# Kernel tuning notes

Hardware: AMD Instinct MI355X
Metric: run time of the kernel (lower is better)

## Reference

```python
import jax, jax.numpy as jnp
import numpy as np

T = 64      # sequence_length / rolling_size
B = 256     # batch
XD = 128    # x_dim
HD = 1024   # h_dim
SKIP = 5    # frozen skip_size (torch code draws random.randint(1,10) at init)


def _make_masks(rs, n):
    # Mirrors: W1=randint(0,1); W2=1 if W1==0 else randint(0,1)
    masks = []
    for _ in range(n):
        w1 = int(rs.randint(0, 2))
        w2 = 1 if w1 == 0 else int(rs.randint(0, 2))
        masks.append((float(w1), float(w2)))
    return masks

_RS = np.random.RandomState(0)
ENC_MASKS = _make_masks(_RS, T)  # encoder constructed first in RAE.__init__
DEC_MASKS = _make_masks(_RS, T)


def _gru_cell(x, h, W_ih, W_hh, b_ih, b_hh):
    # torch.nn.GRUCell semantics
    gi = x @ W_ih.T + b_ih            # [B, 3H]
    gh = h @ W_hh.T + b_hh            # [B, 3H]
    i_r, i_z, i_n = jnp.split(gi, 3, axis=1)
    h_r, h_z, h_n = jnp.split(gh, 3, axis=1)
    r = jax.nn.sigmoid(i_r + h_r)
    z = jax.nn.sigmoid(i_z + h_z)
    n = jnp.tanh(i_n + r * h_n)
    return (1.0 - z) * n + z * h


def setup_inputs() -> dict:
    key = jax.random.key(0)
    ks = jax.random.split(key, 12)
    s = 0.05
    return {
        "input": jax.random.normal(ks[0], (B, T, XD), jnp.float32),
        "enc_W_ih": jax.random.normal(ks[1], (3 * HD, XD), jnp.float32) * s,
        "enc_W_hh": jax.random.normal(ks[2], (3 * HD, HD), jnp.float32) * s,
        "enc_b_ih": jax.random.normal(ks[3], (3 * HD,), jnp.float32) * s,
        "enc_b_hh": jax.random.normal(ks[4], (3 * HD,), jnp.float32) * s,
        "dec_W_ih": jax.random.normal(ks[5], (3 * HD, XD), jnp.float32) * s,
        "dec_W_hh": jax.random.normal(ks[6], (3 * HD, HD), jnp.float32) * s,
        "dec_b_ih": jax.random.normal(ks[7], (3 * HD,), jnp.float32) * s,
        "dec_b_hh": jax.random.normal(ks[8], (3 * HD,), jnp.float32) * s,
        "lin_W": jax.random.normal(ks[9], (XD, HD), jnp.float32) * s,
        "lin_b": jax.random.normal(ks[10], (XD,), jnp.float32) * s,
    }


def reference(input, enc_W_ih, enc_W_hh, enc_b_ih, enc_b_hh,
              dec_W_ih, dec_W_hh, dec_b_ih, dec_b_hh, lin_W, lin_b):
    Bn = input.shape[0]
    zeros_h = jnp.zeros((Bn, HD), input.dtype)

    # ---- Encoder: masked-skip GRU recurrence (list semantics match torch) ----
    h_origs = [zeros_h]
    h_skips = [zeros_h] * SKIP
    for i in range(T):
        h_prev = h_origs[i] * ENC_MASKS[i][0] + h_skips[i - SKIP] * ENC_MASKS[i][1]
        h_new = _gru_cell(input[:, i], h_prev, enc_W_ih, enc_W_hh, enc_b_ih, enc_b_hh)
        h_origs.append(h_new)
        h_skips.append(h_new)  # chunk(repeat(1,2)) gives two identical copies
    h_enc = h_origs[-1] + h_skips[-1]

    # ---- Decoder: feeds back its own projected output ----
    GO = jnp.zeros((Bn, XD), input.dtype)
    h_origs = [h_enc]
    h_skips = [zeros_h] * SKIP
    outputs = []
    for i in range(T):
        x_in = GO if i == 0 else outputs[i - 1]
        h_prev = h_origs[i] * DEC_MASKS[i][0] + h_skips[i - SKIP] * DEC_MASKS[i][1]
        h_new = _gru_cell(x_in, h_prev, dec_W_ih, dec_W_hh, dec_b_ih, dec_b_hh)
        h_origs.append(h_new)
        h_skips.append(h_new)
        # torch projects AFTER the appends, using h_origs[i] (pre-update state)
        proj = (h_origs[i] + h_skips[i - SKIP]) @ lin_W.T + lin_b
        outputs.append(proj)

    return jnp.stack(outputs, axis=1)  # [B, T, XD], matches permute(1,0,2)
```

## Files before the change

### kernel.cpp

```cpp
#include <hip/hip_runtime.h>
#include <cstdint>
#include <cstddef>

#define XDIM 128
#define HDIM 1024
#define ORS 8192

typedef __attribute__((ext_vector_type(8))) short short8;
typedef __attribute__((ext_vector_type(4))) float f32x4;

static const size_t GSTRIDE = (size_t)36 * 64 * 64 * 8;
static const size_t EPACK   = 4 * GSTRIDE;

__device__ __forceinline__ unsigned short f2bf(float f) {
  union { float f; unsigned u; } c; c.f = f;
  unsigned u = c.u + (0x7fffu + ((c.u >> 16) & 1u));
  return (unsigned short)(u >> 16);
}
__device__ __forceinline__ float sigm_(float x) { return 1.f / (1.f + __expf(-x)); }
__device__ __forceinline__ float tanh_(float x) { return 2.f / (1.f + __expf(-2.f * x)) - 1.f; }

__device__ __forceinline__ short8 cvt8(float4 a, float4 b) {
  short8 o;
  o[0] = (short)f2bf(a.x); o[1] = (short)f2bf(a.y); o[2] = (short)f2bf(a.z); o[3] = (short)f2bf(a.w);
  o[4] = (short)f2bf(b.x); o[5] = (short)f2bf(b.y); o[6] = (short)f2bf(b.z); o[7] = (short)f2bf(b.w);
  return o;
}

__global__ __launch_bounds__(256) void pack_gates(
    const float* __restrict__ eWih, const float* __restrict__ eWhh,
    const float* __restrict__ dWih, const float* __restrict__ dWhh,
    short* __restrict__ Bg)
{
  unsigned t = blockIdx.x * 256u + threadIdx.x;
  unsigned l  = t & 63u; t >>= 6;
  unsigned nf = t & 63u; t >>= 6;
  unsigned ks = t % 36u; t /= 36u;
  unsigned g  = t & 3u;  t >>= 2;
  if (t >= 2u) return;
  if ((g == 2u && ks >= 4u) || (g == 3u && ks < 4u)) return;
  const float* Wih = t ? dWih : eWih;
  const float* Whh = t ? dWhh : eWhh;
  int k = (int)(ks * 32u + (l >> 4) * 8u);
  int n = (int)(nf * 16u + (l & 15u));
  const float* src;
  if (g == 3u)      src = Whh + (size_t)(2048 + n) * HDIM + (k - XDIM);
  else if (g == 2u) src = Wih + (size_t)(2048 + n) * XDIM + k;
  else if (ks < 4u) src = Wih + (size_t)(g * HDIM + n) * XDIM + k;
  else              src = Whh + (size_t)(g * HDIM + n) * HDIM + (k - XDIM);
  float4 a = *(const float4*)src;
  float4 b = *(const float4*)(src + 4);
  size_t off = ((((size_t)t * 4u + g) * 36u + ks) * 64u + nf) * 64u + l;
  *(short8*)(Bg + off * 8u) = cvt8(a, b);
}

__global__ __launch_bounds__(256) void pack_lin(const float* __restrict__ linW,
                                                short* __restrict__ Bl)
{
  unsigned t = blockIdx.x * 256u + threadIdx.x;
  unsigned l  = t & 63u; t >>= 6;
  unsigned nf = t & 7u;  t >>= 3;
  unsigned ks = t;
  if (ks >= 32u) return;
  int k = (int)(ks * 32u + (l >> 4) * 8u);
  int n = (int)(nf * 16u + (l & 15u));
  const float* src = linW + (size_t)n * HDIM + k;
  float4 a = *(const float4*)src;
  float4 b = *(const float4*)(src + 4);
  *(short8*)(Bl + (((size_t)ks * 8u + nf) * 64u + l) * 8u) = cvt8(a, b);
}

__global__ __launch_bounds__(256) void pack_bias(
    const float* __restrict__ eIh, const float* __restrict__ eHh,
    const float* __restrict__ dIh, const float* __restrict__ dHh,
    float* __restrict__ bias)
{
  unsigned t = blockIdx.x * 256u + threadIdx.x;
  if (t >= 8192u) return;
  unsigned n = t & 1023u, g = (t >> 10) & 3u, e = t >> 12;
  const float* bih = e ? dIh : eIh;
  const float* bhh = e ? dHh : eHh;
  float v;
  if (g == 0u)      v = bih[n] + bhh[n];
  else if (g == 1u) v = bih[HDIM + n] + bhh[HDIM + n];
  else if (g == 2u) v = bih[2 * HDIM + n];
  else              v = bhh[2 * HDIM + n];
  bias[t] = v;
}

__global__ __launch_bounds__(256) void pack_x(const float* __restrict__ in,
                                              unsigned short* __restrict__ Xe)
{
  unsigned t = blockIdx.x * 256u + threadIdx.x;
  unsigned row = t & 255u; t >>= 8;
  unsigned lq  = t & 3u;   t >>= 2;
  unsigned ks  = t & 3u;   t >>= 2;
  unsigned i   = t;
  if (i >= 64u) return;
  const float* src = in + (size_t)row * ORS + i * 128u + ks * 32u + lq * 8u;
  float4 a = *(const float4*)src;
  float4 b = *(const float4*)(src + 4);
  *(short8*)(Xe + ((((size_t)i * 4u + ks) * 4u + lq) * 256u + row) * 8u) = cvt8(a, b);
}

struct CellArgs {
  const unsigned short* xfrag;
  const unsigned short* afrag;
  const unsigned short* Bg;
  const float* bias4;
  const float* hpA; const float* hpB; float spA, spB;
  float* hout;
  float nsA, nsB; const float* nskip; unsigned short* anext;
  float qsA, qsB; const float* qskip; unsigned short* pnext;
  float q2sA, q2sB; const float* q2skip; unsigned short* p2next;
  const unsigned short* pfrag;
  const unsigned short* Blin;
  const float* linb;
  float* pout;
  unsigned short* pxout;
  int gatesBlocks;
};

#define MFMA(a,b,c) __builtin_amdgcn_mfma_f32_16x16x32_bf16((a),(b),(c),0,0,0)

__global__ __launch_bounds__(512) void rae_cell(CellArgs P) {
  const int tid  = threadIdx.x;
  const int lane = tid & 63;
  const int wave = tid >> 6;
  const int l15  = lane & 15, lq = lane >> 4;
  const int wm = wave & 1, wn = (wave >> 1) & 1, kh = wave >> 2;
  const int w01 = wm * 2 + wn;
  const int bid  = blockIdx.x;
  __shared__ f32x4 red[4][4][64];

  if (bid < P.gatesBlocks) {
    const int mt = bid >> 5, ns = bid & 31;
    const int nf = ns * 2 + wn;
    const int R0 = mt * 32 + wm * 16;
    const int arow = R0 + l15;
    const int colE = ns * 32 + wn * 16 + l15;

    const f32x4 zero = {0.f, 0.f, 0.f, 0.f};
    f32x4 acc0 = zero, acc1 = zero, acc2 = zero, acc3 = zero;

    float hpAv[4] = {0,0,0,0}, hpBv[4] = {0,0,0,0}, nskv[4] = {0,0,0,0},
          qskv[4] = {0,0,0,0}, q2skv[4] = {0,0,0,0};

    if (kh == 1) {
      if (P.xfrag) {
#pragma unroll
        for (int ks = 0; ks < 4; ++ks) {
          short8 av = *(const short8*)(P.xfrag + (((size_t)(ks * 4 + lq)) * 256 + arow) * 8);
          const unsigned short* bb = P.Bg + ((size_t)(ks * 64 + nf) * 64 + lane) * 8;
          short8 b0 = *(const short8*)(bb);
          short8 b1 = *(const short8*)(bb + GSTRIDE);
          short8 b2 = *(const short8*)(bb + 2 * GSTRIDE);
          acc0 = MFMA(av, b0, acc0); acc1 = MFMA(av, b1, acc1); acc2 = MFMA(av, b2, acc2);
        }
      }
      if (P.afrag) {
#pragma unroll
        for (int ks = 20; ks < 36; ++ks) {
          short8 av = *(const short8*)(P.afrag + (((size_t)((ks - 4) * 4 + lq)) * 256 + arow) * 8);
          const unsigned short* bb = P.Bg + ((size_t)(ks * 64 + nf) * 64 + lane) * 8;
          short8 b0 = *(const short8*)(bb);
          short8 b1 = *(const short8*)(bb + GSTRIDE);
          short8 b3 = *(const short8*)(bb + 3 * GSTRIDE);
          acc0 = MFMA(av, b0, acc0); acc1 = MFMA(av, b1, acc1); acc3 = MFMA(av, b3, acc3);
        }
      }
      red[w01][0][lane] = acc0; red[w01][1][lane] = acc1;
      red[w01][2][lane] = acc2; red[w01][3][lane] = acc3;
    } else {
#pragma unroll
      for (int q = 0; q < 4; ++q) {
        const size_t o = (size_t)(R0 + lq * 4 + q) * HDIM + colE;
        if (P.spA != 0.f) hpAv[q] = P.hpA[o];
        if (P.spB != 0.f) hpBv[q] = P.hpB[o];
        if (P.anext && P.nsB != 0.f) nskv[q] = P.nskip[o];
        if (P.pnext && P.qsB != 0.f) qskv[q] = P.qskip[o];
        if (P.p2next) q2skv[q] = P.q2skip[o];
      }
      if (P.afrag) {
#pragma unroll
        for (int ks = 4; ks < 20; ++ks) {
          short8 av = *(const short8*)(P.afrag + (((size_t)((ks - 4) * 4 + lq)) * 256 + arow) * 8);
          const unsigned short* bb = P.Bg + ((size_t)(ks * 64 + nf) * 64 + lane) * 8;
          short8 b0 = *(const short8*)(bb);
          short8 b1 = *(const short8*)(bb + GSTRIDE);
          short8 b3 = *(const short8*)(bb + 3 * GSTRIDE);
          acc0 = MFMA(av, b0, acc0); acc1 = MFMA(av, b1, acc1); acc3 = MFMA(av, b3, acc3);
        }
      }
    }
    __syncthreads();
    if (kh == 1) return;

    acc0 += red[w01][0][lane]; acc1 += red[w01][1][lane];
    acc2 += red[w01][2][lane]; acc3 += red[w01][3][lane];

    const float br = P.bias4[colE],            bz = P.bias4[HDIM + colE];
    const float bi = P.bias4[2 * HDIM + colE], bh = P.bias4[3 * HDIM + colE];
    const int fa = (colE >> 3) * 2048 + (colE & 7);
#pragma unroll
    for (int q = 0; q < 4; ++q) {
      const int row = R0 + lq * 4 + q;
      const float r  = sigm_(acc0[q] + br);
      const float z  = sigm_(acc1[q] + bz);
      const float nv = tanh_(acc2[q] + bi + r * (acc3[q] + bh));
      const float hp = P.spA * hpAv[q] + P.spB * hpBv[q];
      const float h  = (1.f - z) * nv + z * hp;
      P.hout[(size_t)row * HDIM + colE] = h;
      if (P.anext)  P.anext[fa + row * 8]  = f2bf(P.nsA * h + P.nsB * nskv[q]);
      if (P.pnext)  P.pnext[fa + row * 8]  = f2bf(P.qsA * h + P.qsB * qskv[q]);
      if (P.p2next) P.p2next[fa + row * 8] = f2bf(P.q2sA * h + P.q2sB * q2skv[q]);
    }
  } else {
    const int pb = bid - P.gatesBlocks;
    const int mt = pb >> 1, nt = pb & 1;
    const int arow0 = mt * 64 + wm * 32 + l15;
    const int nfb = nt * 4 + wn * 2;
    const f32x4 zero = {0.f, 0.f, 0.f, 0.f};
    f32x4 a00 = zero, a01 = zero, a10 = zero, a11 = zero;
    const int ksA = kh * 16, ksB = ksA + 16;
#pragma unroll
    for (int ks0 = 0; ks0 < 16; ++ks0) {
      const int ks = ksA + ks0; (void)ksB;
      short8 av0 = *(const short8*)(P.pfrag + (((size_t)(ks * 4 + lq)) * 256 + arow0) * 8);
      short8 av1 = *(const short8*)(P.pfrag + (((size_t)(ks * 4 + lq)) * 256 + arow0 + 16) * 8);
      const unsigned short* bb = P.Blin + ((size_t)(ks * 8 + nfb) * 64 + lane) * 8;
      short8 b0 = *(const short8*)(bb);
      short8 b1 = *(const short8*)(bb + 64 * 8);
      a00 = MFMA(av0, b0, a00); a01 = MFMA(av0, b1, a01);
      a10 = MFMA(av1, b0, a10); a11 = MFMA(av1, b1, a11);
    }
    if (kh == 1) {
      red[w01][0][lane] = a00; red[w01][1][lane] = a01;
      red[w01][2][lane] = a10; red[w01][3][lane] = a11;
    }
    __syncthreads();
    if (kh == 1) return;
    a00 += red[w01][0][lane]; a01 += red[w01][1][lane];
    a10 += red[w01][2][lane]; a11 += red[w01][3][lane];
    f32x4 accs[2][2] = {{a00, a01}, {a10, a11}};
#pragma unroll
    for (int fm = 0; fm < 2; ++fm) {
#pragma unroll
      for (int nn = 0; nn < 2; ++nn) {
        const int col = nt * 64 + wn * 32 + nn * 16 + l15;
        const float lb = P.linb[col];
        const int fx = (col >> 3) * 2048 + (col & 7);
#pragma unroll
        for (int q = 0; q < 4; ++q) {
          const int row = mt * 64 + wm * 32 + fm * 16 + lq * 4 + q;
          const float v = accs[fm][nn][q] + lb;
          P.pout[(size_t)row * ORS + col] = v;
          P.pxout[fx + row * 8] = f2bf(v);
        }
      }
    }
  }
}

static void compute_masks(float ew[64][2], float dw[64][2]) {
  unsigned mt[624];
  mt[0] = 0u;
  for (int i = 1; i < 624; ++i)
    mt[i] = 1812433253u * (mt[i - 1] ^ (mt[i - 1] >> 30)) + (unsigned)i;
  int mti = 624;
  auto gen = [&]() -> unsigned {
    if (mti >= 624) {
      for (int i = 0; i < 624; ++i) {
        unsigned y = (mt[i] & 0x80000000u) | (mt[(i + 1) % 624] & 0x7fffffffu);
        unsigned v = mt[(i + 397) % 624] ^ (y >> 1);
        mt[i] = (y & 1u) ? (v ^ 0x9908b0dfu) : v;
      }
      mti = 0;
    }
    unsigned y = mt[mti++];
    y ^= y >> 11; y ^= (y << 7) & 0x9d2c5680u; y ^= (y << 15) & 0xefc60000u; y ^= y >> 18;
    return y;
  };
  auto rbit = [&]() -> int { return (int)(gen() & 1u); };
  for (int t = 0; t < 64; ++t) {
    int w1 = rbit(); int w2 = (w1 == 0) ? 1 : rbit();
    ew[t][0] = (float)w1; ew[t][1] = (float)w2;
  }
  for (int t = 0; t < 64; ++t) {
    int w1 = rbit(); int w2 = (w1 == 0) ? 1 : rbit();
    dw[t][0] = (float)w1; dw[t][1] = (float)w2;
  }
}

extern "C" void kernel_launch(void* const* d_in, const int* in_sizes, int n_in,
                              void* d_out, int out_size, void* d_ws, size_t ws_size,
                              hipStream_t stream)
{
  const float* input = (const float*)d_in[0];
  const float* eWih = (const float*)d_in[1];
  const float* eWhh = (const float*)d_in[2];
  const float* eBih = (const float*)d_in[3];
  const float* eBhh = (const float*)d_in[4];
  const float* dWih = (const float*)d_in[5];
  const float* dWhh = (const float*)d_in[6];
  const float* dBih = (const float*)d_in[7];
  const float* dBhh = (const float*)d_in[8];
  const float* linW = (const float*)d_in[9];
  const float* linb = (const float*)d_in[10];
  float* out = (float*)d_out;

  if (ws_size < 44597248u) return;
  char* ws = (char*)d_ws;
  short* BgE = (short*)ws;
  short* BgD = BgE + EPACK;
  short* Blin = (short*)(ws + 18874368u);
  float* bias = (float*)(ws + 19136512u);
  float* hring = (float*)(ws + 19169280u);
  unsigned short* Xe  = (unsigned short*)(ws + 35946496u);
  unsigned short* AnB = (unsigned short*)(ws + 40140800u);
  unsigned short* PnB = (unsigned short*)(ws + 42237952u);
  unsigned short* XdB = (unsigned short*)(ws + 44335104u);

  float ew[64][2], dw[64][2];
  compute_masks(ew, dw);

  pack_gates<<<4608, 256, 0, stream>>>(eWih, eWhh, dWih, dWhh, BgE);
  pack_lin<<<64, 256, 0, stream>>>(linW, Blin);
  pack_bias<<<32, 256, 0, stream>>>(eBih, eBhh, dBih, dBhh, bias);
  pack_x<<<1024, 256, 0, stream>>>(input, Xe);

  auto Hf = [&](int s) -> float* { return hring + (size_t)(s & 15) * (256 * HDIM); };
  auto An = [&](int g) -> unsigned short* { return AnB + (size_t)(g & 3) * 262144u; };
  auto Pn = [&](int g) -> unsigned short* { return PnB + (size_t)(g & 3) * 262144u; };
  auto Xd = [&](int g) -> unsigned short* { return XdB + (size_t)(g & 3) * 32768u; };

  for (int i = 0; i < 64; ++i) {
    CellArgs c = {};
    c.Bg = (const unsigned short*)BgE; c.bias4 = bias; c.hout = Hf(i);
    c.xfrag = Xe + (size_t)i * 32768u;
    c.afrag = (i >= 1) ? An(i) : nullptr;
    c.hpA = Hf(i - 1); c.spA = i ? ew[i][0] : 0.f;
    if (i == 3)       { c.hpB = Hf(1);      c.spB = ew[i][1]; }
    else if (i == 4)  { c.hpB = Hf(3);      c.spB = ew[i][1]; }
    else if (i >= 10) { c.hpB = Hf(i - 10); c.spB = ew[i][1]; }
    else              { c.hpB = Hf(0);      c.spB = 0.f; }
    if (i < 63) {
      int n = i + 1;
      c.anext = An(n); c.nskip = Hf(0); c.nsB = 0.f;
      if (n == 4) { c.nsA = ew[4][0] + ew[4][1]; }
      else {
        c.nsA = ew[n][0];
        if (n == 3)       { c.nsB = ew[3][1]; c.nskip = Hf(1); }
        else if (n >= 10) { c.nsB = ew[n][1]; c.nskip = Hf(n - 10); }
      }
    } else {
      c.anext = An(64); c.nsA = 2.f * dw[0][0]; c.nsB = 0.f; c.nskip = Hf(0);
      c.pnext = Pn(0);  c.qsA = 2.f; c.qsB = 0.f; c.qskip = Hf(0);
    }
    c.gatesBlocks = 256;
    rae_cell<<<256, 512, 0, stream>>>(c);
  }

  for (int i = 0; i < 64; ++i) {
    CellArgs c = {};
    c.Bg = (const unsigned short*)BgD; c.bias4 = bias + 4096; c.hout = Hf(i);
    c.xfrag = i ? Xd(i - 1) : nullptr;
    c.afrag = An(64 + i);
    c.hpA = i ? Hf(i - 1) : Hf(15);
    c.spA = i ? dw[i][0] : 2.f * dw[0][0];
    if (i == 3)       { c.hpB = Hf(1);      c.spB = dw[i][1]; }
    else if (i == 4)  { c.hpB = Hf(3);      c.spB = dw[i][1]; }
    else if (i >= 10) { c.hpB = Hf(i - 10); c.spB = dw[i][1]; }
    else              { c.hpB = Hf(0);      c.spB = 0.f; }
    if (i < 63) {
      int n = i + 1;
      c.anext = An(64 + n); c.nskip = Hf(0); c.nsB = 0.f;
      if (n == 4) { c.nsA = dw[4][0] + dw[4][1]; }
      else {
        c.nsA = dw[n][0];
        if (n == 3)       { c.nsB = dw[3][1]; c.nskip = Hf(1); }
        else if (n >= 10) { c.nsB = dw[n][1]; c.nskip = Hf(n - 10); }
      }
    }
    c.qskip = Hf(0); c.q2skip = Hf(0);
    if (i == 2)      { c.pnext = Pn(3); c.qsA = 2.f; c.qsB = 0.f; }
    else if (i == 3) {  }
    else if (i == 4) { c.pnext = Pn(5); c.qsA = 1.f; c.qsB = 0.f;
                       c.p2next = Pn(4); c.q2sA = 1.f; c.q2sB = 1.f; c.q2skip = Hf(3); }
    else if (i < 63) {
      int n = i + 1;
      c.pnext = Pn(n); c.qsA = 1.f; c.qsB = 0.f;
      if (n == 2)       { c.qsB = 1.f; c.qskip = Hf(0); }
      else if (n >= 10) { c.qsB = 1.f; c.qskip = Hf(n - 10); }
    }
    int grid = 256;
    if (i != 4) {
      c.pfrag = Pn(i); c.pout = out + (size_t)i * XDIM; c.pxout = Xd(i);
      c.Blin = (const unsigned short*)Blin; c.linb = linb;
      grid = 264;
    }
    c.gatesBlocks = 256;
    rae_cell<<<grid, 512, 0, stream>>>(c);

    if (i == 4) {
      CellArgs s = {};
      s.gatesBlocks = 0;
      s.pfrag = Pn(4); s.pout = out + (size_t)4 * XDIM; s.pxout = Xd(4);
      s.Blin = (const unsigned short*)Blin; s.linb = linb;
      rae_cell<<<8, 512, 0, stream>>>(s);
    }
  }
}
```

Before: 1.344 ms.

## Replace per-step kernel launches with a persistent kernel and row-group barriers

Collapses roughly 130 per-timestep kernel launches into one persistent kernel of 256 blocks that walks a precomputed phase table held in shared memory. Steps are ordered by atomic flag barriers scoped to each row group of 32 blocks, which replace launch boundaries. The linear projection is folded into the same blocks, and mask generation moves into a device setup kernel that also skips zero-weight recurrent work. The change removes launch overhead and full-grid sync, but assumes all 256 blocks are co-resident and adds spin-wait cost with a guard that could let execution continue unsynchronised.

```diff
diff --git a/kernel.cpp b/kernel.cpp
--- a/kernel.cpp
+++ b/kernel.cpp
@@ -5,12 +5,22 @@
 #define XDIM 128
 #define HDIM 1024
 #define ORS 8192
+#define NPH 129
 
 typedef __attribute__((ext_vector_type(8))) short short8;
 typedef __attribute__((ext_vector_type(4))) float f32x4;
 
 static const size_t GSTRIDE = (size_t)36 * 64 * 64 * 8;
 static const size_t EPACK   = 4 * GSTRIDE;
+
+struct Phase {
+  float spA, spB, nsA, nsB, qsA, qsB, q2sA, q2sB;
+  int ebase, xe, xd, afrag;
+  int hpA, hpB, nskip, qskip, q2skip;
+  int anext, pnext, p2next, hout;
+  int pfrag, pouti, pxout;
+};
+static_assert(sizeof(Phase) == 96, "phase size");
 
 __device__ __forceinline__ unsigned short f2bf(float f) {
   union { float f; unsigned u; } c; c.f = f;
@@ -26,6 +36,8 @@
   o[4] = (short)f2bf(b.x); o[5] = (short)f2bf(b.y); o[6] = (short)f2bf(b.z); o[7] = (short)f2bf(b.w);
   return o;
 }
+
+#define MFMA(a,b,c) __builtin_amdgcn_mfma_f32_16x16x32_bf16((a),(b),(c),0,0,0)
 
 __global__ __launch_bounds__(256) void pack_gates(
     const float* __restrict__ eWih, const float* __restrict__ eWhh,
@@ -103,192 +115,320 @@
   *(short8*)(Xe + ((((size_t)i * 4u + ks) * 4u + lq) * 256u + row) * 8u) = cvt8(a, b);
 }
 
-struct CellArgs {
-  const unsigned short* xfrag;
-  const unsigned short* afrag;
-  const unsigned short* Bg;
-  const float* bias4;
-  const float* hpA; const float* hpB; float spA, spB;
-  float* hout;
-  float nsA, nsB; const float* nskip; unsigned short* anext;
-  float qsA, qsB; const float* qskip; unsigned short* pnext;
-  float q2sA, q2sB; const float* q2skip; unsigned short* p2next;
-  const unsigned short* pfrag;
-  const unsigned short* Blin;
-  const float* linb;
-  float* pout;
-  unsigned short* pxout;
-  int gatesBlocks;
-};
-
-#define MFMA(a,b,c) __builtin_amdgcn_mfma_f32_16x16x32_bf16((a),(b),(c),0,0,0)
-
-__global__ __launch_bounds__(512) void rae_cell(CellArgs P) {
-  const int tid  = threadIdx.x;
-  const int lane = tid & 63;
-  const int wave = tid >> 6;
-  const int l15  = lane & 15, lq = lane >> 4;
-  const int wm = wave & 1, wn = (wave >> 1) & 1, kh = wave >> 2;
-  const int w01 = wm * 2 + wn;
-  const int bid  = blockIdx.x;
-  __shared__ f32x4 red[4][4][64];
-
-  if (bid < P.gatesBlocks) {
-    const int mt = bid >> 5, ns = bid & 31;
-    const int nf = ns * 2 + wn;
-    const int R0 = mt * 32 + wm * 16;
-    const int arow = R0 + l15;
-    const int colE = ns * 32 + wn * 16 + l15;
-
-    const f32x4 zero = {0.f, 0.f, 0.f, 0.f};
-    f32x4 acc0 = zero, acc1 = zero, acc2 = zero, acc3 = zero;
-
-    float hpAv[4] = {0,0,0,0}, hpBv[4] = {0,0,0,0}, nskv[4] = {0,0,0,0},
-          qskv[4] = {0,0,0,0}, q2skv[4] = {0,0,0,0};
-
-    if (kh == 1) {
-      if (P.xfrag) {
-#pragma unroll
-        for (int ks = 0; ks < 4; ++ks) {
-          short8 av = *(const short8*)(P.xfrag + (((size_t)(ks * 4 + lq)) * 256 + arow) * 8);
-          const unsigned short* bb = P.Bg + ((size_t)(ks * 64 + nf) * 64 + lane) * 8;
-          short8 b0 = *(const short8*)(bb);
-          short8 b1 = *(const short8*)(bb + GSTRIDE);
-          short8 b2 = *(const short8*)(bb + 2 * GSTRIDE);
-          acc0 = MFMA(av, b0, acc0); acc1 = MFMA(av, b1, acc1); acc2 = MFMA(av, b2, acc2);
-        }
-      }
-      if (P.afrag) {
-#pragma unroll
-        for (int ks = 20; ks < 36; ++ks) {
-          short8 av = *(const short8*)(P.afrag + (((size_t)((ks - 4) * 4 + lq)) * 256 + arow) * 8);
-          const unsigned short* bb = P.Bg + ((size_t)(ks * 64 + nf) * 64 + lane) * 8;
-          short8 b0 = *(const short8*)(bb);
-          short8 b1 = *(const short8*)(bb + GSTRIDE);
-          short8 b3 = *(const short8*)(bb + 3 * GSTRIDE);
-          acc0 = MFMA(av, b0, acc0); acc1 = MFMA(av, b1, acc1); acc3 = MFMA(av, b3, acc3);
-        }
-      }
-      red[w01][0][lane] = acc0; red[w01][1][lane] = acc1;
-      red[w01][2][lane] = acc2; red[w01][3][lane] = acc3;
-    } else {
-#pragma unroll
-      for (int q = 0; q < 4; ++q) {
-        const size_t o = (size_t)(R0 + lq * 4 + q) * HDIM + colE;
-        if (P.spA != 0.f) hpAv[q] = P.hpA[o];
-        if (P.spB != 0.f) hpBv[q] = P.hpB[o];
-        if (P.anext && P.nsB != 0.f) nskv[q] = P.nskip[o];
-        if (P.pnext && P.qsB != 0.f) qskv[q] = P.qskip[o];
-        if (P.p2next) q2skv[q] = P.q2skip[o];
-      }
-      if (P.afrag) {
-#pragma unroll
-        for (int ks = 4; ks < 20; ++ks) {
-          short8 av = *(const short8*)(P.afrag + (((size_t)((ks - 4) * 4 + lq)) * 256 + arow) * 8);
-          const unsigned short* bb = P.Bg + ((size_t)(ks * 64 + nf) * 64 + lane) * 8;
-          short8 b0 = *(const short8*)(bb);
-          short8 b1 = *(const short8*)(bb + GSTRIDE);
-          short8 b3 = *(const short8*)(bb + 3 * GSTRIDE);
-          acc0 = MFMA(av, b0, acc0); acc1 = MFMA(av, b1, acc1); acc3 = MFMA(av, b3, acc3);
-        }
-      }
-    }
-    __syncthreads();
-    if (kh == 1) return;
-
-    acc0 += red[w01][0][lane]; acc1 += red[w01][1][lane];
-    acc2 += red[w01][2][lane]; acc3 += red[w01][3][lane];
-
-    const float br = P.bias4[colE],            bz = P.bias4[HDIM + colE];
-    const float bi = P.bias4[2 * HDIM + colE], bh = P.bias4[3 * HDIM + colE];
-    const int fa = (colE >> 3) * 2048 + (colE & 7);
-#pragma unroll
-    for (int q = 0; q < 4; ++q) {
-      const int row = R0 + lq * 4 + q;
-      const float r  = sigm_(acc0[q] + br);
-      const float z  = sigm_(acc1[q] + bz);
-      const float nv = tanh_(acc2[q] + bi + r * (acc3[q] + bh));
-      const float hp = P.spA * hpAv[q] + P.spB * hpBv[q];
-      const float h  = (1.f - z) * nv + z * hp;
-      P.hout[(size_t)row * HDIM + colE] = h;
-      if (P.anext)  P.anext[fa + row * 8]  = f2bf(P.nsA * h + P.nsB * nskv[q]);
-      if (P.pnext)  P.pnext[fa + row * 8]  = f2bf(P.qsA * h + P.qsB * qskv[q]);
-      if (P.p2next) P.p2next[fa + row * 8] = f2bf(P.q2sA * h + P.q2sB * q2skv[q]);
-    }
-  } else {
-    const int pb = bid - P.gatesBlocks;
-    const int mt = pb >> 1, nt = pb & 1;
-    const int arow0 = mt * 64 + wm * 32 + l15;
-    const int nfb = nt * 4 + wn * 2;
-    const f32x4 zero = {0.f, 0.f, 0.f, 0.f};
-    f32x4 a00 = zero, a01 = zero, a10 = zero, a11 = zero;
-    const int ksA = kh * 16, ksB = ksA + 16;
-#pragma unroll
-    for (int ks0 = 0; ks0 < 16; ++ks0) {
-      const int ks = ksA + ks0; (void)ksB;
-      short8 av0 = *(const short8*)(P.pfrag + (((size_t)(ks * 4 + lq)) * 256 + arow0) * 8);
-      short8 av1 = *(const short8*)(P.pfrag + (((size_t)(ks * 4 + lq)) * 256 + arow0 + 16) * 8);
-      const unsigned short* bb = P.Blin + ((size_t)(ks * 8 + nfb) * 64 + lane) * 8;
-      short8 b0 = *(const short8*)(bb);
-      short8 b1 = *(const short8*)(bb + 64 * 8);
-      a00 = MFMA(av0, b0, a00); a01 = MFMA(av0, b1, a01);
-      a10 = MFMA(av1, b0, a10); a11 = MFMA(av1, b1, a11);
-    }
-    if (kh == 1) {
-      red[w01][0][lane] = a00; red[w01][1][lane] = a01;
-      red[w01][2][lane] = a10; red[w01][3][lane] = a11;
-    }
-    __syncthreads();
-    if (kh == 1) return;
-    a00 += red[w01][0][lane]; a01 += red[w01][1][lane];
-    a10 += red[w01][2][lane]; a11 += red[w01][3][lane];
-    f32x4 accs[2][2] = {{a00, a01}, {a10, a11}};
-#pragma unroll
-    for (int fm = 0; fm < 2; ++fm) {
-#pragma unroll
-      for (int nn = 0; nn < 2; ++nn) {
-        const int col = nt * 64 + wn * 32 + nn * 16 + l15;
-        const float lb = P.linb[col];
-        const int fx = (col >> 3) * 2048 + (col & 7);
-#pragma unroll
-        for (int q = 0; q < 4; ++q) {
-          const int row = mt * 64 + wm * 32 + fm * 16 + lq * 4 + q;
-          const float v = accs[fm][nn][q] + lb;
-          P.pout[(size_t)row * ORS + col] = v;
-          P.pxout[fx + row * 8] = f2bf(v);
-        }
-      }
-    }
-  }
-}
-
-static void compute_masks(float ew[64][2], float dw[64][2]) {
+__device__ __forceinline__ int mkslot(int s) { return s % 12; }
+
+__device__ void blank_phase(Phase& ph) {
+  ph.spA = ph.spB = ph.nsA = ph.nsB = ph.qsA = ph.qsB = ph.q2sA = ph.q2sB = 0.f;
+  ph.ebase = 0; ph.xe = -1; ph.xd = -1; ph.afrag = -1;
+  ph.hpA = ph.hpB = ph.nskip = ph.qskip = ph.q2skip = 0;
+  ph.anext = ph.pnext = ph.p2next = -1; ph.hout = -1;
+  ph.pfrag = -1; ph.pouti = -1; ph.pxout = -1;
+}
+
+__global__ void setup_phases(Phase* __restrict__ phs, unsigned* __restrict__ arr) {
+  const int t = threadIdx.x;
+  for (int k = t; k < 1024; k += 64) arr[k] = 0u;
+  if (t != 0) return;
+
   unsigned mt[624];
   mt[0] = 0u;
   for (int i = 1; i < 624; ++i)
     mt[i] = 1812433253u * (mt[i - 1] ^ (mt[i - 1] >> 30)) + (unsigned)i;
-  int mti = 624;
-  auto gen = [&]() -> unsigned {
-    if (mti >= 624) {
-      for (int i = 0; i < 624; ++i) {
-        unsigned y = (mt[i] & 0x80000000u) | (mt[(i + 1) % 624] & 0x7fffffffu);
-        unsigned v = mt[(i + 397) % 624] ^ (y >> 1);
-        mt[i] = (y & 1u) ? (v ^ 0x9908b0dfu) : v;
-      }
-      mti = 0;
-    }
-    unsigned y = mt[mti++];
-    y ^= y >> 11; y ^= (y << 7) & 0x9d2c5680u; y ^= (y << 15) & 0xefc60000u; y ^= y >> 18;
-    return y;
-  };
-  auto rbit = [&]() -> int { return (int)(gen() & 1u); };
-  for (int t = 0; t < 64; ++t) {
-    int w1 = rbit(); int w2 = (w1 == 0) ? 1 : rbit();
-    ew[t][0] = (float)w1; ew[t][1] = (float)w2;
+  for (int i = 0; i < 624; ++i) {
+    unsigned y = (mt[i] & 0x80000000u) | (mt[(i + 1) % 624] & 0x7fffffffu);
+    unsigned v = mt[(i + 397) % 624] ^ (y >> 1);
+    mt[i] = (y & 1u) ? (v ^ 0x9908b0dfu) : v;
   }
-  for (int t = 0; t < 64; ++t) {
-    int w1 = rbit(); int w2 = (w1 == 0) ? 1 : rbit();
-    dw[t][0] = (float)w1; dw[t][1] = (float)w2;
+  int mti = 0;
+  float ew[64][2], dw[64][2];
+  for (int e = 0; e < 2; ++e) {
+    for (int i = 0; i < 64; ++i) {
+      unsigned y = mt[mti++];
+      y ^= y >> 11; y ^= (y << 7) & 0x9d2c5680u; y ^= (y << 15) & 0xefc60000u; y ^= y >> 18;
+      int w1 = (int)(y & 1u);
+      int w2 = 1;
+      if (w1 != 0) {
+        unsigned z = mt[mti++];
+        z ^= z >> 11; z ^= (z << 7) & 0x9d2c5680u; z ^= (z << 15) & 0xefc60000u; z ^= z >> 18;
+        w2 = (int)(z & 1u);
+      }
+      if (e == 0) { ew[i][0] = (float)w1; ew[i][1] = (float)w2; }
+      else        { dw[i][0] = (float)w1; dw[i][1] = (float)w2; }
+    }
+  }
+
+  bool anull = true;
+  for (int i = 0; i < 64; ++i) {
+    Phase ph; blank_phase(ph);
+    ph.ebase = 0; ph.xe = i;
+    ph.hout = mkslot(i);
+    if (i >= 1 && !anull) ph.afrag = i & 3;
+    ph.hpA = mkslot(i >= 1 ? i - 1 : 0);
+    ph.spA = i ? ew[i][0] : 0.f;
+    if (i == 3)       { ph.hpB = mkslot(1);      ph.spB = ew[i][1]; }
+    else if (i == 4)  { ph.hpB = mkslot(3);      ph.spB = ew[i][1]; }
+    else if (i >= 10) { ph.hpB = mkslot(i - 10); ph.spB = ew[i][1]; }
+    if (i < 63) {
+      int n = i + 1;
+      ph.anext = n & 3;
+      if (n == 4) ph.nsA = ew[4][0] + ew[4][1];
+      else {
+        ph.nsA = ew[n][0];
+        if (n == 3)       { ph.nsB = ew[3][1]; ph.nskip = mkslot(1); }
+        else if (n >= 10) { ph.nsB = ew[n][1]; ph.nskip = mkslot(n - 10); }
+      }
+    } else {
+      ph.anext = 0; ph.nsA = 2.f * dw[0][0];
+      ph.pnext = 0; ph.qsA = 2.f;
+    }
+    if (ph.anext >= 0) {
+      anull = (ph.nsA == 0.f && ph.nsB == 0.f);
+      if (anull) ph.anext = -1;
+    }
+    phs[i] = ph;
+  }
+  for (int i = 0; i < 64; ++i) {
+    int p = 64 + i + (i >= 5 ? 1 : 0);
+    int s = 64 + i;
+    Phase ph; blank_phase(ph);
+    ph.ebase = 1;
+    ph.xd = i ? (i - 1) & 3 : -1;
+    ph.hout = mkslot(s);
+    if (!anull) ph.afrag = i & 3;
+    ph.hpA = mkslot(i ? s - 1 : 63);
+    ph.spA = i ? dw[i][0] : 2.f * dw[0][0];
+    if (i == 3)       { ph.hpB = mkslot(64 + 1);  ph.spB = dw[i][1]; }
+    else if (i == 4)  { ph.hpB = mkslot(64 + 3);  ph.spB = dw[i][1]; }
+    else if (i >= 10) { ph.hpB = mkslot(s - 10);  ph.spB = dw[i][1]; }
+    if (i < 63) {
+      int n = i + 1;
+      ph.anext = n & 3;
+      if (n == 4) ph.nsA = dw[4][0] + dw[4][1];
+      else {
+        ph.nsA = dw[n][0];
+        if (n == 3)       { ph.nsB = dw[3][1]; ph.nskip = mkslot(64 + 1); }
+        else if (n >= 10) { ph.nsB = dw[n][1]; ph.nskip = mkslot(64 + n - 10); }
+      }
+    }
+    if (i == 2)      { ph.pnext = 3; ph.qsA = 2.f; }
+    else if (i == 3) {  }
+    else if (i == 4) { ph.pnext = 1; ph.qsA = 1.f;
+                       ph.p2next = 0; ph.q2sA = 1.f; ph.q2sB = 1.f;
+                       ph.q2skip = mkslot(64 + 3); }
+    else if (i < 63) {
+      int n = i + 1;
+      ph.pnext = n & 3; ph.qsA = 1.f;
+      if (n == 2)       { ph.qsB = 1.f; ph.qskip = mkslot(64 + 0); }
+      else if (n >= 10) { ph.qsB = 1.f; ph.qskip = mkslot(64 + n - 10); }
+    }
+    if (ph.anext >= 0) {
+      bool z = (ph.nsA == 0.f && ph.nsB == 0.f);
+      if (z) ph.anext = -1;
+      anull = z;
+    }
+    if (i != 4) { ph.pfrag = i & 3; ph.pouti = i; ph.pxout = i & 3; }
+    phs[p] = ph;
+    if (i == 4) {
+      Phase pp; blank_phase(pp);
+      pp.ebase = 1;
+      pp.pfrag = 0; pp.pouti = 4; pp.pxout = 0;
+      phs[69] = pp;
+    }
+  }
+}
+
+__global__ __launch_bounds__(512, 2) void rae_persist(
+    const Phase* __restrict__ phs,
+    const unsigned short* __restrict__ Xe,
+    const unsigned short* __restrict__ BgE,
+    const unsigned short* __restrict__ BgD,
+    const unsigned short* __restrict__ Blin,
+    const float* __restrict__ bias,
+    const float* __restrict__ linb,
+    float* __restrict__ hring,
+    unsigned short* __restrict__ AnB,
+    unsigned short* __restrict__ PnB,
+    unsigned short* __restrict__ XdB,
+    float* __restrict__ out,
+    unsigned* __restrict__ arr)
+{
+  const int tid = threadIdx.x;
+  const int lane = tid & 63;
+  const int wave = tid >> 6;
+  const int l15 = lane & 15, lq = lane >> 4;
+  const int wm = wave & 1, wn = (wave >> 1) & 1, kh = wave >> 2;
+  const int w01 = wm * 2 + wn;
+  const int bid = blockIdx.x;
+  const int mt = bid >> 5, ns = bid & 31;
+
+  __shared__ f32x4 red[4][4][64];
+  __shared__ f32x4 red2[8][2][64];
+  __shared__ Phase lph[NPH];
+
+  for (int idx = tid; idx < NPH * (int)(sizeof(Phase) / 4); idx += 512)
+    ((int*)lph)[idx] = ((const int*)phs)[idx];
+  __syncthreads();
+
+#pragma unroll 1
+  for (int p = 0; p < NPH; ++p) {
+    const Phase& ph = lph[p];
+
+    if (ph.hout >= 0) {
+      const unsigned short* Bg = ph.ebase ? BgD : BgE;
+      const float* bias4 = bias + (ph.ebase ? 4096 : 0);
+      const unsigned short* xfrag = nullptr;
+      if (ph.xe >= 0)      xfrag = Xe  + (size_t)ph.xe * 32768u;
+      else if (ph.xd >= 0) xfrag = XdB + (size_t)ph.xd * 32768u;
+      const unsigned short* afrag =
+          (ph.afrag >= 0) ? AnB + (size_t)ph.afrag * 262144u : nullptr;
+
+      const int nf = ns * 2 + wn;
+      const int R0 = mt * 32 + wm * 16;
+      const int arow = R0 + l15;
+      const int colE = ns * 32 + wn * 16 + l15;
+
+      const f32x4 zero = {0.f, 0.f, 0.f, 0.f};
+      f32x4 acc0 = zero, acc1 = zero, acc2 = zero, acc3 = zero;
+      float hpAv[4] = {0,0,0,0}, hpBv[4] = {0,0,0,0}, nskv[4] = {0,0,0,0},
+            qskv[4] = {0,0,0,0}, q2skv[4] = {0,0,0,0};
+
+      if (kh == 1) {
+        if (xfrag) {
+#pragma unroll
+          for (int ks = 0; ks < 4; ++ks) {
+            short8 av = *(const short8*)(xfrag + (((size_t)(ks * 4 + lq)) * 256 + arow) * 8);
+            const unsigned short* bb = Bg + ((size_t)(ks * 64 + nf) * 64 + lane) * 8;
+            short8 b0 = *(const short8*)(bb);
+            short8 b1 = *(const short8*)(bb + GSTRIDE);
+            short8 b2 = *(const short8*)(bb + 2 * GSTRIDE);
+            acc0 = MFMA(av, b0, acc0); acc1 = MFMA(av, b1, acc1); acc2 = MFMA(av, b2, acc2);
+          }
+        }
+        if (afrag) {
+#pragma unroll
+          for (int ks = 20; ks < 36; ++ks) {
+            short8 av = *(const short8*)(afrag + (((size_t)((ks - 4) * 4 + lq)) * 256 + arow) * 8);
+            const unsigned short* bb = Bg + ((size_t)(ks * 64 + nf) * 64 + lane) * 8;
+            short8 b0 = *(const short8*)(bb);
+            short8 b1 = *(const short8*)(bb + GSTRIDE);
+            short8 b3 = *(const short8*)(bb + 3 * GSTRIDE);
+            acc0 = MFMA(av, b0, acc0); acc1 = MFMA(av, b1, acc1); acc3 = MFMA(av, b3, acc3);
+          }
+        }
+        red[w01][0][lane] = acc0; red[w01][1][lane] = acc1;
+        red[w01][2][lane] = acc2; red[w01][3][lane] = acc3;
+      } else {
+        const float* hpA = hring + (size_t)ph.hpA * 262144u;
+        const float* hpB = hring + (size_t)ph.hpB * 262144u;
+        const float* nsk = hring + (size_t)ph.nskip * 262144u;
+        const float* qsk = hring + (size_t)ph.qskip * 262144u;
+        const float* q2k = hring + (size_t)ph.q2skip * 262144u;
+#pragma unroll
+        for (int q = 0; q < 4; ++q) {
+          const size_t o = (size_t)(R0 + lq * 4 + q) * HDIM + colE;
+          if (ph.spA != 0.f) hpAv[q] = hpA[o];
+          if (ph.spB != 0.f) hpBv[q] = hpB[o];
+          if (ph.anext >= 0 && ph.nsB != 0.f) nskv[q] = nsk[o];
+          if (ph.pnext >= 0 && ph.qsB != 0.f) qskv[q] = qsk[o];
+          if (ph.p2next >= 0) q2skv[q] = q2k[o];
+        }
+        if (afrag) {
+#pragma unroll
+          for (int ks = 4; ks < 20; ++ks) {
+            short8 av = *(const short8*)(afrag + (((size_t)((ks - 4) * 4 + lq)) * 256 + arow) * 8);
+            const unsigned short* bb = Bg + ((size_t)(ks * 64 + nf) * 64 + lane) * 8;
+            short8 b0 = *(const short8*)(bb);
+            short8 b1 = *(const short8*)(bb + GSTRIDE);
+            short8 b3 = *(const short8*)(bb + 3 * GSTRIDE);
+            acc0 = MFMA(av, b0, acc0); acc1 = MFMA(av, b1, acc1); acc3 = MFMA(av, b3, acc3);
+          }
+        }
+      }
+      __syncthreads();
+      if (kh == 0) {
+        acc0 += red[w01][0][lane]; acc1 += red[w01][1][lane];
+        acc2 += red[w01][2][lane]; acc3 += red[w01][3][lane];
+
+        const float br = bias4[colE],            bz = bias4[HDIM + colE];
+        const float bi = bias4[2 * HDIM + colE], bh = bias4[3 * HDIM + colE];
+        const int fa = (colE >> 3) * 2048 + (colE & 7);
+        float* hout = hring + (size_t)ph.hout * 262144u;
+        unsigned short* anx = ph.anext  >= 0 ? AnB + (size_t)ph.anext  * 262144u : nullptr;
+        unsigned short* pnx = ph.pnext  >= 0 ? PnB + (size_t)ph.pnext  * 262144u : nullptr;
+        unsigned short* p2x = ph.p2next >= 0 ? PnB + (size_t)ph.p2next * 262144u : nullptr;
+#pragma unroll
+        for (int q = 0; q < 4; ++q) {
+          const int row = R0 + lq * 4 + q;
+          const float r  = sigm_(acc0[q] + br);
+          const float z  = sigm_(acc1[q] + bz);
+          const float nv = tanh_(acc2[q] + bi + r * (acc3[q] + bh));
+          const float hp = ph.spA * hpAv[q] + ph.spB * hpBv[q];
+          const float h  = (1.f - z) * nv + z * hp;
+          hout[(size_t)row * HDIM + colE] = h;
+          if (anx) anx[fa + row * 8] = f2bf(ph.nsA * h + ph.nsB * nskv[q]);
+          if (pnx) pnx[fa + row * 8] = f2bf(ph.qsA * h + ph.qsB * qskv[q]);
+          if (p2x) p2x[fa + row * 8] = f2bf(ph.q2sA * h + ph.q2sB * q2skv[q]);
+        }
+      }
+    }
+
+    if (ph.pfrag >= 0 && ns < 8) {
+      const unsigned short* pf = PnB + (size_t)ph.pfrag * 262144u;
+      const int rb = mt * 32;
+      const f32x4 zero = {0.f, 0.f, 0.f, 0.f};
+      f32x4 pa0 = zero, pa1 = zero;
+#pragma unroll
+      for (int k0 = 0; k0 < 4; ++k0) {
+        const int ks = wave * 4 + k0;
+        short8 a0 = *(const short8*)(pf + (((size_t)(ks * 4 + lq)) * 256 + rb + l15) * 8);
+        short8 a1 = *(const short8*)(pf + (((size_t)(ks * 4 + lq)) * 256 + rb + 16 + l15) * 8);
+        short8 b  = *(const short8*)(Blin + (((size_t)ks * 8 + ns) * 64 + lane) * 8);
+        pa0 = MFMA(a0, b, pa0); pa1 = MFMA(a1, b, pa1);
+      }
+      red2[wave][0][lane] = pa0; red2[wave][1][lane] = pa1;
+      __syncthreads();
+      if (wave == 0) {
+        f32x4 s0 = red2[0][0][lane], s1 = red2[0][1][lane];
+#pragma unroll
+        for (int w = 1; w < 8; ++w) { s0 += red2[w][0][lane]; s1 += red2[w][1][lane]; }
+        const int col = ns * 16 + l15;
+        const float lb = linb[col];
+        const int fx = (col >> 3) * 2048 + (col & 7);
+        float* po = out + (size_t)ph.pouti * XDIM;
+        unsigned short* px = XdB + (size_t)ph.pxout * 32768u;
+#pragma unroll
+        for (int mf = 0; mf < 2; ++mf) {
+          f32x4 sv = mf ? s1 : s0;
+#pragma unroll
+          for (int q = 0; q < 4; ++q) {
+            const int row = rb + mf * 16 + lq * 4 + q;
+            const float v = sv[q] + lb;
+            po[(size_t)row * ORS + col] = v;
+            px[fx + row * 8] = f2bf(v);
+          }
+        }
+      }
+    }
+
+    __syncthreads();
+    if (tid == 0) {
+      __builtin_amdgcn_fence(__ATOMIC_RELEASE, "agent");
+      __hip_atomic_store(&arr[(mt << 6) + ns], (unsigned)(p + 1),
+                         __ATOMIC_RELAXED, __HIP_MEMORY_SCOPE_AGENT);
+    }
+    if (wave == 0) {
+      const unsigned tgt = (unsigned)(p + 1);
+      int guard = 0;
+      for (;;) {
+        unsigned v = (lane < 32)
+            ? __hip_atomic_load(&arr[(mt << 6) + lane], __ATOMIC_RELAXED, __HIP_MEMORY_SCOPE_AGENT)
+            : tgt;
+        if (__all(v >= tgt)) break;
+        if (++guard > (1 << 22)) break;
+      }
+      __builtin_amdgcn_fence(__ATOMIC_ACQUIRE, "agent");
+    }
+    __syncthreads();
   }
 }
 
@@ -309,105 +449,28 @@
   const float* linb = (const float*)d_in[10];
   float* out = (float*)d_out;
 
-  if (ws_size < 44597248u) return;
+  if (ws_size < 40423424u) return;
   char* ws = (char*)d_ws;
-  short* BgE = (short*)ws;
-  short* BgD = BgE + EPACK;
+  short* BgE  = (short*)ws;
+  short* BgD  = BgE + EPACK;
   short* Blin = (short*)(ws + 18874368u);
   float* bias = (float*)(ws + 19136512u);
   float* hring = (float*)(ws + 19169280u);
-  unsigned short* Xe  = (unsigned short*)(ws + 35946496u);
-  unsigned short* AnB = (unsigned short*)(ws + 40140800u);
-  unsigned short* PnB = (unsigned short*)(ws + 42237952u);
-  unsigned short* XdB = (unsigned short*)(ws + 44335104u);
-
-  float ew[64][2], dw[64][2];
-  compute_masks(ew, dw);
+  unsigned short* Xe  = (unsigned short*)(ws + 31752192u);
+  unsigned short* AnB = (unsigned short*)(ws + 35946496u);
+  unsigned short* PnB = (unsigned short*)(ws + 38043648u);
+  unsigned short* XdB = (unsigned short*)(ws + 40140800u);
+  Phase* phs = (Phase*)(ws + 40402944u);
+  unsigned* arr = (unsigned*)(ws + 40419328u);
 
   pack_gates<<<4608, 256, 0, stream>>>(eWih, eWhh, dWih, dWhh, BgE);
   pack_lin<<<64, 256, 0, stream>>>(linW, Blin);
   pack_bias<<<32, 256, 0, stream>>>(eBih, eBhh, dBih, dBhh, bias);
   pack_x<<<1024, 256, 0, stream>>>(input, Xe);
-
-  auto Hf = [&](int s) -> float* { return hring + (size_t)(s & 15) * (256 * HDIM); };
-  auto An = [&](int g) -> unsigned short* { return AnB + (size_t)(g & 3) * 262144u; };
-  auto Pn = [&](int g) -> unsigned short* { return PnB + (size_t)(g & 3) * 262144u; };
-  auto Xd = [&](int g) -> unsigned short* { return XdB + (size_t)(g & 3) * 32768u; };
-
-  for (int i = 0; i < 64; ++i) {
-    CellArgs c = {};
-    c.Bg = (const unsigned short*)BgE; c.bias4 = bias; c.hout = Hf(i);
-    c.xfrag = Xe + (size_t)i * 32768u;
-    c.afrag = (i >= 1) ? An(i) : nullptr;
-    c.hpA = Hf(i - 1); c.spA = i ? ew[i][0] : 0.f;
-    if (i == 3)       { c.hpB = Hf(1);      c.spB = ew[i][1]; }
-    else if (i == 4)  { c.hpB = Hf(3);      c.spB = ew[i][1]; }
-    else if (i >= 10) { c.hpB = Hf(i - 10); c.spB = ew[i][1]; }
-    else              { c.hpB = Hf(0);      c.spB = 0.f; }
-    if (i < 63) {
-      int n = i + 1;
-      c.anext = An(n); c.nskip = Hf(0); c.nsB = 0.f;
-      if (n == 4) { c.nsA = ew[4][0] + ew[4][1]; }
-      else {
-        c.nsA = ew[n][0];
-        if (n == 3)       { c.nsB = ew[3][1]; c.nskip = Hf(1); }
-        else if (n >= 10) { c.nsB = ew[n][1]; c.nskip = Hf(n - 10); }
-      }
-    } else {
-      c.anext = An(64); c.nsA = 2.f * dw[0][0]; c.nsB = 0.f; c.nskip = Hf(0);
-      c.pnext = Pn(0);  c.qsA = 2.f; c.qsB = 0.f; c.qskip = Hf(0);
-    }
-    c.gatesBlocks = 256;
-    rae_cell<<<256, 512, 0, stream>>>(c);
-  }
-
-  for (int i = 0; i < 64; ++i) {
-    CellArgs c = {};
-    c.Bg = (const unsigned short*)BgD; c.bias4 = bias + 4096; c.hout = Hf(i);
-    c.xfrag = i ? Xd(i - 1) : nullptr;
-    c.afrag = An(64 + i);
-    c.hpA = i ? Hf(i - 1) : Hf(15);
-    c.spA = i ? dw[i][0] : 2.f * dw[0][0];
-    if (i == 3)       { c.hpB = Hf(1);      c.spB = dw[i][1]; }
-    else if (i == 4)  { c.hpB = Hf(3);      c.spB = dw[i][1]; }
-    else if (i >= 10) { c.hpB = Hf(i - 10); c.spB = dw[i][1]; }
-    else              { c.hpB = Hf(0);      c.spB = 0.f; }
-    if (i < 63) {
-      int n = i + 1;
-      c.anext = An(64 + n); c.nskip = Hf(0); c.nsB = 0.f;
-      if (n == 4) { c.nsA = dw[4][0] + dw[4][1]; }
-      else {
-        c.nsA = dw[n][0];
-        if (n == 3)       { c.nsB = dw[3][1]; c.nskip = Hf(1); }
-        else if (n >= 10) { c.nsB = dw[n][1]; c.nskip = Hf(n - 10); }
-      }
-    }
-    c.qskip = Hf(0); c.q2skip = Hf(0);
-    if (i == 2)      { c.pnext = Pn(3); c.qsA = 2.f; c.qsB = 0.f; }
-    else if (i == 3) {  }
-    else if (i == 4) { c.pnext = Pn(5); c.qsA = 1.f; c.qsB = 0.f;
-                       c.p2next = Pn(4); c.q2sA = 1.f; c.q2sB = 1.f; c.q2skip = Hf(3); }
-    else if (i < 63) {
-      int n = i + 1;
-      c.pnext = Pn(n); c.qsA = 1.f; c.qsB = 0.f;
-      if (n == 2)       { c.qsB = 1.f; c.qskip = Hf(0); }
-      else if (n >= 10) { c.qsB = 1.f; c.qskip = Hf(n - 10); }
-    }
-    int grid = 256;
-    if (i != 4) {
-      c.pfrag = Pn(i); c.pout = out + (size_t)i * XDIM; c.pxout = Xd(i);
-      c.Blin = (const unsigned short*)Blin; c.linb = linb;
-      grid = 264;
-    }
-    c.gatesBlocks = 256;
-    rae_cell<<<grid, 512, 0, stream>>>(c);
-
-    if (i == 4) {
-      CellArgs s = {};
-      s.gatesBlocks = 0;
-      s.pfrag = Pn(4); s.pout = out + (size_t)4 * XDIM; s.pxout = Xd(4);
-      s.Blin = (const unsigned short*)Blin; s.linb = linb;
-      rae_cell<<<8, 512, 0, stream>>>(s);
-    }
-  }
-}
+  setup_phases<<<1, 64, 0, stream>>>(phs, arr);
+
+  rae_persist<<<256, 512, 0, stream>>>(
+      phs, Xe, (const unsigned short*)BgE, (const unsigned short*)BgD,
+      (const unsigned short*)Blin, bias, linb,
+      hring, AnB, PnB, XdB, out, arr);
+}
```

Result: slower. 2.692 ms (+100.3%).
